# Optimization experiments

Hardware: AMD Instinct MI355X
Metric: run time of the kernel (lower is better)

Reference implementation:

```python
import jax, jax.numpy as jnp
import numpy as np

N = 262144
D = 3            # n_dims
G = 128          # n_gaussians
F = 128          # n_features
L = 8            # num_positional_encoding_terms
H = 512          # nodes_per_layer
OUT = 1          # n_outputs
PE_DIM = L * 2 * D  # 48
IN0 = PE_DIM + F    # 176


def setup_inputs() -> dict:
    key = jax.random.key(0)
    ks = jax.random.split(key, 16)
    x = jax.random.uniform(ks[0], (N, D), dtype=jnp.float32) * 2.0 - 1.0
    centers = jax.random.uniform(ks[1], (G, D), dtype=jnp.float32) * 2.0 - 1.0
    # diagonal covariances (as in the torch init: eye * rand), kept well-conditioned
    diag = 0.05 + 0.1 * jax.random.uniform(ks[2], (G, D), dtype=jnp.float32)
    cov = jax.vmap(jnp.diag)(diag)  # [G, D, D]
    bnd = np.sqrt(6.0 / F) / 30.0
    gfeat = jax.random.uniform(ks[3], (G, F), dtype=jnp.float32, minval=-bnd, maxval=bnd)

    def lin(kw, kb, fan_out, fan_in, scale):
        W = jax.random.uniform(kw, (fan_out, fan_in), dtype=jnp.float32, minval=-scale, maxval=scale)
        b = jax.random.uniform(kb, (fan_out,), dtype=jnp.float32, minval=-scale, maxval=scale)
        return W, b

    W1, b1 = lin(ks[4], ks[5], H, IN0, float(np.sqrt(6.0 / IN0)))          # LReLU layer
    sine_s = float(np.sqrt(6.0 / H) / 30.0)
    W2, b2 = lin(ks[6], ks[7], H, H, sine_s)
    W3, b3 = lin(ks[8], ks[9], H, H, sine_s)
    W4, b4 = lin(ks[10], ks[11], H, H, sine_s)
    W5, b5 = lin(ks[12], ks[13], OUT, H, float(np.sqrt(2.0 / (H + OUT))))  # final linear
    return {"x": x, "centers": centers, "cov": cov, "gfeat": gfeat,
            "W1": W1, "b1": b1, "W2": W2, "b2": b2, "W3": W3, "b3": b3,
            "W4": W4, "b4": b4, "W5": W5, "b5": b5}


def _positional_encoding(x):
    # torch layout: for each freq l, [sin(2^l*pi*x), sin(..y), sin(..z), cos(..x), cos(..y), cos(..z)]
    freqs = (2.0 ** jnp.arange(L, dtype=jnp.float32)) * jnp.pi  # [L]
    s = x[:, None, :] * freqs[None, :, None]                    # [N, L, D]
    pe = jnp.concatenate([jnp.sin(s), jnp.cos(s)], axis=-1)     # [N, L, 2D]
    return pe.reshape(x.shape[0], L * 2 * D)


def reference(x, centers, cov, gfeat, W1, b1, W2, b2, W3, b3, W4, b4, W5, b5):
    pe = _positional_encoding(x)                                # [N, 48]
    # Gaussian mixture density per point per gaussian
    inv = jnp.linalg.inv(cov)                                   # [G, D, D]
    det = jnp.linalg.det(cov)                                   # [G]
    coeff = 1.0 / (((2.0 * jnp.pi) ** (D / 2.0)) * jnp.sqrt(det))  # [G]
    diff = x[:, None, :] - centers[None, :, :]                  # [N, G, D]
    maha = jnp.einsum('ngd,gde,nge->ng', diff, inv, diff)       # [N, G]
    dens = coeff[None, :] * jnp.exp(-0.5 * maha)                # [N, G]
    feat = dens @ gfeat                                         # [N, F]
    h = jnp.concatenate([feat, pe], axis=1)                     # [N, 176]
    h = jax.nn.leaky_relu(h @ W1.T + b1, 0.2)
    h = jnp.sin(30.0 * (h @ W2.T + b2))
    h = jnp.sin(30.0 * (h @ W3.T + b3))
    h = jnp.sin(30.0 * (h @ W4.T + b4))
    return h @ W5.T + b5                                        # [N, 1]
```

## Files before the change

kernel.cpp:

```cpp
#include <hip/hip_runtime.h>

typedef __attribute__((ext_vector_type(8))) short bf16x8;
typedef __attribute__((ext_vector_type(4))) float f32x4;

#define NPTS 262144
#define PTS_PER_BLK 128
#define TPB 512

__device__ __forceinline__ unsigned short f2bf(float f) {
  unsigned int u = __float_as_uint(f);
  u += 0x7fffu + ((u >> 16) & 1u);
  return (unsigned short)(u >> 16);
}
__device__ __forceinline__ float bf2f(unsigned short s) {
  return __uint_as_float(((unsigned int)s) << 16);
}

__global__ void prep_w(const float* __restrict__ src, unsigned short* __restrict__ dst,
                       int KIN, int KB, int trans, int OUTD, int total) {
  int idx = blockIdx.x * blockDim.x + threadIdx.x;
  if (idx >= total) return;
  int i = idx & 7;
  int l = (idx >> 3) & 63;
  int t = idx >> 9;
  int kb = t % KB, nb = t / KB;
  int row = nb * 16 + (l & 15);
  int k = kb * 32 + (l >> 4) * 8 + i;
  float v = 0.0f;
  if (k < KIN) v = trans ? src[k * OUTD + row] : src[row * KIN + k];
  dst[idx] = f2bf(v);
}

__global__ void prep_gauss(const float* __restrict__ centers, const float* __restrict__ cov,
                           float* __restrict__ gp) {
  int g = threadIdx.x;
  if (g >= 128) return;
  float c0 = cov[g * 9 + 0], c1 = cov[g * 9 + 4], c2 = cov[g * 9 + 8];
  float det = c0 * c1 * c2;
  float coeff = 1.0f / (15.749609945722419f * sqrtf(det));
  gp[g * 8 + 0] = centers[g * 3 + 0];
  gp[g * 8 + 1] = centers[g * 3 + 1];
  gp[g * 8 + 2] = centers[g * 3 + 2];
  gp[g * 8 + 3] = 1.0f / c0;
  gp[g * 8 + 4] = 1.0f / c1;
  gp[g * 8 + 5] = 1.0f / c2;
  gp[g * 8 + 6] = coeff;
  gp[g * 8 + 7] = 0.0f;
}


template <int KB, int ACT>
__device__ __forceinline__ void mlp_layer(const unsigned short* __restrict__ wf,
                                          const float* __restrict__ bias,
                                          char* hb, int lane, int wid) {
  const int r8 = lane >> 4, l15 = lane & 15;
  f32x4 acc[4][8];
#pragma unroll
  for (int a0 = 0; a0 < 4; ++a0)
#pragma unroll
    for (int b0 = 0; b0 < 8; ++b0)
      acc[a0][b0] = (f32x4){0.f, 0.f, 0.f, 0.f};

  const unsigned short* wbase = wf + wid * 4 * KB * 512 + lane * 8;
#pragma unroll 4
  for (int kb = 0; kb < KB; ++kb) {
    bf16x8 a[4];
#pragma unroll
    for (int nf = 0; nf < 4; ++nf)
      a[nf] = *(const bf16x8*)(wbase + (nf * KB + kb) * 512);
    bf16x8 b[8];
#pragma unroll
    for (int pf = 0; pf < 8; ++pf) {
      int pt = pf * 16 + l15;
      int off = (pt * 1024 + kb * 64 + r8 * 16) ^ ((pt & 7) << 4);
      b[pf] = *(const bf16x8*)(hb + off);
    }
#pragma unroll
    for (int nf = 0; nf < 4; ++nf)
#pragma unroll
      for (int pf = 0; pf < 8; ++pf)
        acc[nf][pf] = __builtin_amdgcn_mfma_f32_16x16x32_bf16(a[nf], b[pf], acc[nf][pf], 0, 0, 0);
  }
  __syncthreads();
#pragma unroll
  for (int nf = 0; nf < 4; ++nf) {
    int n0 = wid * 64 + nf * 16 + r8 * 4;
    f32x4 bv = *(const f32x4*)(bias + n0);
#pragma unroll
    for (int pf = 0; pf < 8; ++pf) {
      int pt = pf * 16 + l15;
      float v[4];
#pragma unroll
      for (int r = 0; r < 4; ++r) {
        float z = acc[nf][pf][r] + bv[r];
        if (ACT == 1) z = (z > 0.f) ? z : 0.2f * z;
        else if (ACT == 2) z = __sinf(30.f * z);
        v[r] = z;
      }
      unsigned long long pk =
          (unsigned long long)((unsigned int)f2bf(v[0]) | ((unsigned int)f2bf(v[1]) << 16)) |
          ((unsigned long long)((unsigned int)f2bf(v[2]) | ((unsigned int)f2bf(v[3]) << 16)) << 32);
      int off = (pt * 1024 + n0 * 2) ^ ((pt & 7) << 4);
      *(unsigned long long*)(hb + off) = pk;
    }
  }
  __syncthreads();
}

__global__ __launch_bounds__(TPB, 2) void gmminr_main(
    const float* __restrict__ x,
    const float* __restrict__ b1, const float* __restrict__ b2,
    const float* __restrict__ b3, const float* __restrict__ b4,
    const float* __restrict__ w5, const float* __restrict__ b5,
    const unsigned short* __restrict__ wf1, const unsigned short* __restrict__ wf2,
    const unsigned short* __restrict__ wf3, const unsigned short* __restrict__ wf4,
    const unsigned short* __restrict__ gff, const float* __restrict__ gp,
    float* __restrict__ out) {
  __shared__ char hb[PTS_PER_BLK * 1024];
  const int tid = threadIdx.x;
  const int lane = tid & 63;
  const int wid = tid >> 6;
  const int pt0 = blockIdx.x * PTS_PER_BLK;

  {
    const int pt = tid >> 2;
    const int q = tid & 3;
    const float X = x[(pt0 + pt) * 3 + 0];
    const float Y = x[(pt0 + pt) * 3 + 1];
    const float Z = x[(pt0 + pt) * 3 + 2];
#pragma unroll 2
    for (int j = 0; j < 32; j += 4) {
      float d4[4];
#pragma unroll
      for (int e = 0; e < 4; ++e) {
        const float* P = gp + (q * 32 + j + e) * 8;
        float dx = X - P[0], dy = Y - P[1], dz = Z - P[2];
        float m = dx * dx * P[3] + dy * dy * P[4] + dz * dz * P[5];
        d4[e] = P[6] * __expf(-0.5f * m);
      }
      unsigned long long pk =
          (unsigned long long)((unsigned int)f2bf(d4[0]) | ((unsigned int)f2bf(d4[1]) << 16)) |
          ((unsigned long long)((unsigned int)f2bf(d4[2]) | ((unsigned int)f2bf(d4[3]) << 16)) << 32);
      int col = 256 + q * 32 + j;
      int off = (pt * 1024 + col * 2) ^ ((pt & 7) << 4);
      *(unsigned long long*)(hb + off) = pk;
    }
    float co[3] = {X, Y, Z};
#pragma unroll
    for (int lg = 0; lg < 2; ++lg) {
      int le = q * 2 + lg;
      float fr = 3.14159265358979323846f * (float)(1 << le);
#pragma unroll
      for (int d = 0; d < 3; ++d) {
        float arg = fr * co[d];
        float s = __sinf(arg), c = __cosf(arg);
        int cs = 128 + le * 6 + d;
        *(unsigned short*)(hb + ((pt * 1024 + cs * 2) ^ ((pt & 7) << 4))) = f2bf(s);
        *(unsigned short*)(hb + ((pt * 1024 + (cs + 3) * 2) ^ ((pt & 7) << 4))) = f2bf(c);
      }
    }
    {
      int col = 176 + q * 4;
      int off = (pt * 1024 + col * 2) ^ ((pt & 7) << 4);
      *(unsigned long long*)(hb + off) = 0ull;
    }
  }
  __syncthreads();

  {
    const int r8 = lane >> 4, l15 = lane & 15;
    f32x4 facc[8];
#pragma unroll
    for (int pf = 0; pf < 8; ++pf) facc[pf] = (f32x4){0.f, 0.f, 0.f, 0.f};
    const unsigned short* gbase = gff + wid * 4 * 512 + lane * 8;
#pragma unroll
    for (int kb = 0; kb < 4; ++kb) {
      bf16x8 a = *(const bf16x8*)(gbase + kb * 512);
#pragma unroll
      for (int pf = 0; pf < 8; ++pf) {
        int pt = pf * 16 + l15;
        int off = (pt * 1024 + 512 + kb * 64 + r8 * 16) ^ ((pt & 7) << 4);
        bf16x8 b = *(const bf16x8*)(hb + off);
        facc[pf] = __builtin_amdgcn_mfma_f32_16x16x32_bf16(a, b, facc[pf], 0, 0, 0);
      }
    }
    int f0 = wid * 16 + r8 * 4;
#pragma unroll
    for (int pf = 0; pf < 8; ++pf) {
      int pt = pf * 16 + l15;
      unsigned long long pk =
          (unsigned long long)((unsigned int)f2bf(facc[pf][0]) | ((unsigned int)f2bf(facc[pf][1]) << 16)) |
          ((unsigned long long)((unsigned int)f2bf(facc[pf][2]) | ((unsigned int)f2bf(facc[pf][3]) << 16)) << 32);
      int off = (pt * 1024 + f0 * 2) ^ ((pt & 7) << 4);
      *(unsigned long long*)(hb + off) = pk;
    }
  }
  __syncthreads();

  mlp_layer<6, 1>(wf1, b1, hb, lane, wid);
  mlp_layer<16, 2>(wf2, b2, hb, lane, wid);
  mlp_layer<16, 2>(wf3, b3, hb, lane, wid);
  mlp_layer<16, 2>(wf4, b4, hb, lane, wid);

  {
    const int pt = tid >> 2, q = tid & 3;
    float s = 0.f;
#pragma unroll 4
    for (int kk = 0; kk < 128; kk += 8) {
      int k = q * 128 + kk;
      int off = (pt * 1024 + k * 2) ^ ((pt & 7) << 4);
      bf16x8 hv = *(const bf16x8*)(hb + off);
      f32x4 w0 = *(const f32x4*)(w5 + k);
      f32x4 w1 = *(const f32x4*)(w5 + k + 4);
#pragma unroll
      for (int e = 0; e < 4; ++e) s += bf2f((unsigned short)hv[e]) * w0[e];
#pragma unroll
      for (int e = 0; e < 4; ++e) s += bf2f((unsigned short)hv[4 + e]) * w1[e];
    }
    s += __shfl_down(s, 2, 4);
    s += __shfl_down(s, 1, 4);
    if (q == 0) out[pt0 + pt] = s + b5[0];
  }
}

extern "C" void kernel_launch(void* const* d_in, const int* in_sizes, int n_in,
                              void* d_out, int out_size, void* d_ws, size_t ws_size,
                              hipStream_t stream) {
  const float* x   = (const float*)d_in[0];
  const float* cen = (const float*)d_in[1];
  const float* cov = (const float*)d_in[2];
  const float* gfe = (const float*)d_in[3];
  const float* W1  = (const float*)d_in[4];
  const float* b1  = (const float*)d_in[5];
  const float* W2  = (const float*)d_in[6];
  const float* b2  = (const float*)d_in[7];
  const float* W3  = (const float*)d_in[8];
  const float* b3  = (const float*)d_in[9];
  const float* W4  = (const float*)d_in[10];
  const float* b4  = (const float*)d_in[11];
  const float* W5  = (const float*)d_in[12];
  const float* b5  = (const float*)d_in[13];
  float* out = (float*)d_out;

  char* ws = (char*)d_ws;
  unsigned short* wf1 = (unsigned short*)(ws);
  unsigned short* wf2 = (unsigned short*)(ws + 196608);
  unsigned short* wf3 = (unsigned short*)(ws + 720896);
  unsigned short* wf4 = (unsigned short*)(ws + 1245184);
  unsigned short* gff = (unsigned short*)(ws + 1769472);
  float* gp = (float*)(ws + 1802240);

  prep_w<<<98304 / 256, 256, 0, stream>>>(W1, wf1, 176, 6, 0, 512, 98304);
  prep_w<<<262144 / 256, 256, 0, stream>>>(W2, wf2, 512, 16, 0, 512, 262144);
  prep_w<<<262144 / 256, 256, 0, stream>>>(W3, wf3, 512, 16, 0, 512, 262144);
  prep_w<<<262144 / 256, 256, 0, stream>>>(W4, wf4, 512, 16, 0, 512, 262144);
  prep_w<<<16384 / 256, 256, 0, stream>>>(gfe, gff, 128, 4, 1, 128, 16384);
  prep_gauss<<<1, 128, 0, stream>>>(cen, cov, gp);

  gmminr_main<<<NPTS / PTS_PER_BLK, TPB, 0, stream>>>(
      x, b1, b2, b3, b4, W5, b5, wf1, wf2, wf3, wf4, gff, gp, out);
}
```

Before: 678.0 us.

## Halve points per block, raise occupancy, fuse last sine layer with output

```diff
diff --git a/kernel.cpp b/kernel.cpp
--- a/kernel.cpp
+++ b/kernel.cpp
@@ -4,16 +4,20 @@
 typedef __attribute__((ext_vector_type(4))) float f32x4;
 
 #define NPTS 262144
-#define PTS_PER_BLK 128
+#define PTS_PER_BLK 64
 #define TPB 512
+#define NBLK (NPTS / PTS_PER_BLK)
 
 __device__ __forceinline__ unsigned short f2bf(float f) {
   unsigned int u = __float_as_uint(f);
   u += 0x7fffu + ((u >> 16) & 1u);
   return (unsigned short)(u >> 16);
 }
-__device__ __forceinline__ float bf2f(unsigned short s) {
-  return __uint_as_float(((unsigned int)s) << 16);
+__device__ __forceinline__ unsigned int pklo(float a, float b) {
+  return (unsigned int)f2bf(a) | ((unsigned int)f2bf(b) << 16);
+}
+__device__ __forceinline__ unsigned long long pk4(float a, float b, float c, float d) {
+  return (unsigned long long)pklo(a, b) | ((unsigned long long)pklo(c, d) << 32);
 }
 
 __global__ void prep_w(const float* __restrict__ src, unsigned short* __restrict__ dst,
@@ -48,29 +52,34 @@
   gp[g * 8 + 7] = 0.0f;
 }
 
+__global__ void prep_scale(const float* __restrict__ src, float* __restrict__ dst, int n) {
+  int i = blockIdx.x * blockDim.x + threadIdx.x;
+  if (i < n) dst[i] = src[i] * 30.0f;
+}
+
 
 template <int KB, int ACT>
 __device__ __forceinline__ void mlp_layer(const unsigned short* __restrict__ wf,
                                           const float* __restrict__ bias,
                                           char* hb, int lane, int wid) {
   const int r8 = lane >> 4, l15 = lane & 15;
-  f32x4 acc[4][8];
+  f32x4 acc[4][4];
 #pragma unroll
   for (int a0 = 0; a0 < 4; ++a0)
 #pragma unroll
-    for (int b0 = 0; b0 < 8; ++b0)
+    for (int b0 = 0; b0 < 4; ++b0)
       acc[a0][b0] = (f32x4){0.f, 0.f, 0.f, 0.f};
 
   const unsigned short* wbase = wf + wid * 4 * KB * 512 + lane * 8;
-#pragma unroll 4
+#pragma unroll 2
   for (int kb = 0; kb < KB; ++kb) {
     bf16x8 a[4];
 #pragma unroll
     for (int nf = 0; nf < 4; ++nf)
       a[nf] = *(const bf16x8*)(wbase + (nf * KB + kb) * 512);
-    bf16x8 b[8];
-#pragma unroll
-    for (int pf = 0; pf < 8; ++pf) {
+    bf16x8 b[4];
+#pragma unroll
+    for (int pf = 0; pf < 4; ++pf) {
       int pt = pf * 16 + l15;
       int off = (pt * 1024 + kb * 64 + r8 * 16) ^ ((pt & 7) << 4);
       b[pf] = *(const bf16x8*)(hb + off);
@@ -78,7 +87,7 @@
 #pragma unroll
     for (int nf = 0; nf < 4; ++nf)
 #pragma unroll
-      for (int pf = 0; pf < 8; ++pf)
+      for (int pf = 0; pf < 4; ++pf)
         acc[nf][pf] = __builtin_amdgcn_mfma_f32_16x16x32_bf16(a[nf], b[pf], acc[nf][pf], 0, 0, 0);
   }
   __syncthreads();
@@ -87,97 +96,81 @@
     int n0 = wid * 64 + nf * 16 + r8 * 4;
     f32x4 bv = *(const f32x4*)(bias + n0);
 #pragma unroll
-    for (int pf = 0; pf < 8; ++pf) {
+    for (int pf = 0; pf < 4; ++pf) {
       int pt = pf * 16 + l15;
-      float v[4];
+      float z[4];
 #pragma unroll
       for (int r = 0; r < 4; ++r) {
-        float z = acc[nf][pf][r] + bv[r];
-        if (ACT == 1) z = (z > 0.f) ? z : 0.2f * z;
-        else if (ACT == 2) z = __sinf(30.f * z);
-        v[r] = z;
-      }
-      unsigned long long pk =
-          (unsigned long long)((unsigned int)f2bf(v[0]) | ((unsigned int)f2bf(v[1]) << 16)) |
-          ((unsigned long long)((unsigned int)f2bf(v[2]) | ((unsigned int)f2bf(v[3]) << 16)) << 32);
+        float t = acc[nf][pf][r];
+        if (ACT == 1) { t += bv[r]; t = t > 0.f ? t : 0.2f * t; }
+        else { t = __sinf(fmaf(t, 30.0f, bv[r])); }
+        z[r] = t;
+      }
       int off = (pt * 1024 + n0 * 2) ^ ((pt & 7) << 4);
-      *(unsigned long long*)(hb + off) = pk;
-    }
-  }
-  __syncthreads();
-}
-
-__global__ __launch_bounds__(TPB, 2) void gmminr_main(
+      *(unsigned long long*)(hb + off) = pk4(z[0], z[1], z[2], z[3]);
+    }
+  }
+  __syncthreads();
+}
+
+__global__ __launch_bounds__(TPB, 4) void gmminr_main(
     const float* __restrict__ x,
-    const float* __restrict__ b1, const float* __restrict__ b2,
-    const float* __restrict__ b3, const float* __restrict__ b4,
+    const float* __restrict__ b1, const float* __restrict__ bs2,
+    const float* __restrict__ bs3, const float* __restrict__ bs4,
     const float* __restrict__ w5, const float* __restrict__ b5,
     const unsigned short* __restrict__ wf1, const unsigned short* __restrict__ wf2,
     const unsigned short* __restrict__ wf3, const unsigned short* __restrict__ wf4,
     const unsigned short* __restrict__ gff, const float* __restrict__ gp,
     float* __restrict__ out) {
-  __shared__ char hb[PTS_PER_BLK * 1024];
+  __shared__ char hb[PTS_PER_BLK * 1024 + 2048];
+  float* part = (float*)(hb + PTS_PER_BLK * 1024);
   const int tid = threadIdx.x;
   const int lane = tid & 63;
   const int wid = tid >> 6;
+  const int r8 = lane >> 4, l15 = lane & 15;
   const int pt0 = blockIdx.x * PTS_PER_BLK;
 
   {
-    const int pt = tid >> 2;
-    const int q = tid & 3;
-    const float X = x[(pt0 + pt) * 3 + 0];
-    const float Y = x[(pt0 + pt) * 3 + 1];
-    const float Z = x[(pt0 + pt) * 3 + 2];
-#pragma unroll 2
-    for (int j = 0; j < 32; j += 4) {
+    const int pt = tid >> 3;
+    const int q = tid & 7;
+    const int gpt = pt0 + pt;
+    const float X = x[gpt * 3 + 0], Y = x[gpt * 3 + 1], Z = x[gpt * 3 + 2];
+    const int ps = (pt & 7) << 4;
+    const int pb = pt * 1024;
+#pragma unroll
+    for (int j = 0; j < 16; j += 4) {
       float d4[4];
 #pragma unroll
       for (int e = 0; e < 4; ++e) {
-        const float* P = gp + (q * 32 + j + e) * 8;
+        const float* P = gp + (q * 16 + j + e) * 8;
         float dx = X - P[0], dy = Y - P[1], dz = Z - P[2];
-        float m = dx * dx * P[3] + dy * dy * P[4] + dz * dz * P[5];
+        float m = fmaf(dx * dx, P[3], fmaf(dy * dy, P[4], dz * dz * P[5]));
         d4[e] = P[6] * __expf(-0.5f * m);
       }
-      unsigned long long pk =
-          (unsigned long long)((unsigned int)f2bf(d4[0]) | ((unsigned int)f2bf(d4[1]) << 16)) |
-          ((unsigned long long)((unsigned int)f2bf(d4[2]) | ((unsigned int)f2bf(d4[3]) << 16)) << 32);
-      int col = 256 + q * 32 + j;
-      int off = (pt * 1024 + col * 2) ^ ((pt & 7) << 4);
-      *(unsigned long long*)(hb + off) = pk;
-    }
-    float co[3] = {X, Y, Z};
-#pragma unroll
-    for (int lg = 0; lg < 2; ++lg) {
-      int le = q * 2 + lg;
-      float fr = 3.14159265358979323846f * (float)(1 << le);
-#pragma unroll
-      for (int d = 0; d < 3; ++d) {
-        float arg = fr * co[d];
-        float s = __sinf(arg), c = __cosf(arg);
-        int cs = 128 + le * 6 + d;
-        *(unsigned short*)(hb + ((pt * 1024 + cs * 2) ^ ((pt & 7) << 4))) = f2bf(s);
-        *(unsigned short*)(hb + ((pt * 1024 + (cs + 3) * 2) ^ ((pt & 7) << 4))) = f2bf(c);
-      }
-    }
-    {
-      int col = 176 + q * 4;
-      int off = (pt * 1024 + col * 2) ^ ((pt & 7) << 4);
-      *(unsigned long long*)(hb + off) = 0ull;
-    }
+      int off = (pb + 512 + q * 32 + j * 2) ^ ps;
+      *(unsigned long long*)(hb + off) = pk4(d4[0], d4[1], d4[2], d4[3]);
+    }
+    float fr = 3.14159265358979323846f * (float)(1 << q);
+    float sx = __sinf(fr * X), sy = __sinf(fr * Y), sz2 = __sinf(fr * Z);
+    float cx = __cosf(fr * X), cy = __cosf(fr * Y), cz = __cosf(fr * Z);
+    int base = pb + 256 + 12 * q;
+    *(unsigned int*)(hb + ((base + 0) ^ ps)) = pklo(sx, sy);
+    *(unsigned int*)(hb + ((base + 4) ^ ps)) = pklo(sz2, cx);
+    *(unsigned int*)(hb + ((base + 8) ^ ps)) = pklo(cy, cz);
+    *(unsigned int*)(hb + ((pb + 352 + 4 * q) ^ ps)) = 0u;
   }
   __syncthreads();
 
   {
-    const int r8 = lane >> 4, l15 = lane & 15;
-    f32x4 facc[8];
-#pragma unroll
-    for (int pf = 0; pf < 8; ++pf) facc[pf] = (f32x4){0.f, 0.f, 0.f, 0.f};
+    f32x4 facc[4];
+#pragma unroll
+    for (int pf = 0; pf < 4; ++pf) facc[pf] = (f32x4){0.f, 0.f, 0.f, 0.f};
     const unsigned short* gbase = gff + wid * 4 * 512 + lane * 8;
 #pragma unroll
     for (int kb = 0; kb < 4; ++kb) {
       bf16x8 a = *(const bf16x8*)(gbase + kb * 512);
 #pragma unroll
-      for (int pf = 0; pf < 8; ++pf) {
+      for (int pf = 0; pf < 4; ++pf) {
         int pt = pf * 16 + l15;
         int off = (pt * 1024 + 512 + kb * 64 + r8 * 16) ^ ((pt & 7) << 4);
         bf16x8 b = *(const bf16x8*)(hb + off);
@@ -186,40 +179,64 @@
     }
     int f0 = wid * 16 + r8 * 4;
 #pragma unroll
-    for (int pf = 0; pf < 8; ++pf) {
+    for (int pf = 0; pf < 4; ++pf) {
       int pt = pf * 16 + l15;
-      unsigned long long pk =
-          (unsigned long long)((unsigned int)f2bf(facc[pf][0]) | ((unsigned int)f2bf(facc[pf][1]) << 16)) |
-          ((unsigned long long)((unsigned int)f2bf(facc[pf][2]) | ((unsigned int)f2bf(facc[pf][3]) << 16)) << 32);
       int off = (pt * 1024 + f0 * 2) ^ ((pt & 7) << 4);
-      *(unsigned long long*)(hb + off) = pk;
+      *(unsigned long long*)(hb + off) = pk4(facc[pf][0], facc[pf][1], facc[pf][2], facc[pf][3]);
     }
   }
   __syncthreads();
 
   mlp_layer<6, 1>(wf1, b1, hb, lane, wid);
-  mlp_layer<16, 2>(wf2, b2, hb, lane, wid);
-  mlp_layer<16, 2>(wf3, b3, hb, lane, wid);
-  mlp_layer<16, 2>(wf4, b4, hb, lane, wid);
+  mlp_layer<16, 2>(wf2, bs2, hb, lane, wid);
+  mlp_layer<16, 2>(wf3, bs3, hb, lane, wid);
 
   {
-    const int pt = tid >> 2, q = tid & 3;
-    float s = 0.f;
-#pragma unroll 4
-    for (int kk = 0; kk < 128; kk += 8) {
-      int k = q * 128 + kk;
-      int off = (pt * 1024 + k * 2) ^ ((pt & 7) << 4);
-      bf16x8 hv = *(const bf16x8*)(hb + off);
-      f32x4 w0 = *(const f32x4*)(w5 + k);
-      f32x4 w1 = *(const f32x4*)(w5 + k + 4);
-#pragma unroll
-      for (int e = 0; e < 4; ++e) s += bf2f((unsigned short)hv[e]) * w0[e];
-#pragma unroll
-      for (int e = 0; e < 4; ++e) s += bf2f((unsigned short)hv[4 + e]) * w1[e];
-    }
-    s += __shfl_down(s, 2, 4);
-    s += __shfl_down(s, 1, 4);
-    if (q == 0) out[pt0 + pt] = s + b5[0];
+    f32x4 acc[4][4];
+#pragma unroll
+    for (int a0 = 0; a0 < 4; ++a0)
+#pragma unroll
+      for (int b0 = 0; b0 < 4; ++b0)
+        acc[a0][b0] = (f32x4){0.f, 0.f, 0.f, 0.f};
+    const unsigned short* wbase = wf4 + wid * 4 * 16 * 512 + lane * 8;
+#pragma unroll 2
+    for (int kb = 0; kb < 16; ++kb) {
+      bf16x8 a[4];
+#pragma unroll
+      for (int nf = 0; nf < 4; ++nf)
+        a[nf] = *(const bf16x8*)(wbase + (nf * 16 + kb) * 512);
+#pragma unroll
+      for (int pf = 0; pf < 4; ++pf) {
+        int pt = pf * 16 + l15;
+        int off = (pt * 1024 + kb * 64 + r8 * 16) ^ ((pt & 7) << 4);
+        bf16x8 b = *(const bf16x8*)(hb + off);
+#pragma unroll
+        for (int nf = 0; nf < 4; ++nf)
+          acc[nf][pf] = __builtin_amdgcn_mfma_f32_16x16x32_bf16(a[nf], b, acc[nf][pf], 0, 0, 0);
+      }
+    }
+#pragma unroll
+    for (int pf = 0; pf < 4; ++pf) {
+      float s = 0.f;
+#pragma unroll
+      for (int nf = 0; nf < 4; ++nf) {
+        int n0 = wid * 64 + nf * 16 + r8 * 4;
+        f32x4 bv = *(const f32x4*)(bs4 + n0);
+        f32x4 wv = *(const f32x4*)(w5 + n0);
+#pragma unroll
+        for (int r = 0; r < 4; ++r)
+          s += __sinf(fmaf(acc[nf][pf][r], 30.0f, bv[r])) * wv[r];
+      }
+      s += __shfl_xor(s, 16);
+      s += __shfl_xor(s, 32);
+      if (lane < 16) part[(pf * 16 + l15) * 8 + wid] = s;
+    }
+  }
+  __syncthreads();
+  if (tid < PTS_PER_BLK) {
+    const f32x4* pp = (const f32x4*)part;
+    f32x4 a = pp[tid * 2], b = pp[tid * 2 + 1];
+    out[pt0 + tid] = a[0] + a[1] + a[2] + a[3] + b[0] + b[1] + b[2] + b[3] + b5[0];
   }
 }
 
@@ -248,15 +265,21 @@
   unsigned short* wf3 = (unsigned short*)(ws + 720896);
   unsigned short* wf4 = (unsigned short*)(ws + 1245184);
   unsigned short* gff = (unsigned short*)(ws + 1769472);
-  float* gp = (float*)(ws + 1802240);
-
-  prep_w<<<98304 / 256, 256, 0, stream>>>(W1, wf1, 176, 6, 0, 512, 98304);
-  prep_w<<<262144 / 256, 256, 0, stream>>>(W2, wf2, 512, 16, 0, 512, 262144);
-  prep_w<<<262144 / 256, 256, 0, stream>>>(W3, wf3, 512, 16, 0, 512, 262144);
-  prep_w<<<262144 / 256, 256, 0, stream>>>(W4, wf4, 512, 16, 0, 512, 262144);
-  prep_w<<<16384 / 256, 256, 0, stream>>>(gfe, gff, 128, 4, 1, 128, 16384);
+  float* gp  = (float*)(ws + 1802240);
+  float* bs2 = (float*)(ws + 1806336);
+  float* bs3 = (float*)(ws + 1808384);
+  float* bs4 = (float*)(ws + 1810432);
+
+  prep_w<<<384, 256, 0, stream>>>(W1, wf1, 176, 6, 0, 512, 98304);
+  prep_w<<<1024, 256, 0, stream>>>(W2, wf2, 512, 16, 0, 512, 262144);
+  prep_w<<<1024, 256, 0, stream>>>(W3, wf3, 512, 16, 0, 512, 262144);
+  prep_w<<<1024, 256, 0, stream>>>(W4, wf4, 512, 16, 0, 512, 262144);
+  prep_w<<<64, 256, 0, stream>>>(gfe, gff, 128, 4, 1, 128, 16384);
   prep_gauss<<<1, 128, 0, stream>>>(cen, cov, gp);
-
-  gmminr_main<<<NPTS / PTS_PER_BLK, TPB, 0, stream>>>(
-      x, b1, b2, b3, b4, W5, b5, wf1, wf2, wf3, wf4, gff, gp, out);
-}
+  prep_scale<<<2, 256, 0, stream>>>(b2, bs2, 512);
+  prep_scale<<<2, 256, 0, stream>>>(b3, bs3, 512);
+  prep_scale<<<2, 256, 0, stream>>>(b4, bs4, 512);
+
+  gmminr_main<<<NBLK, TPB, 0, stream>>>(x, b1, bs2, bs3, bs4, W5, b5,
+                                        wf1, wf2, wf3, wf4, gff, gp, out);
+}
```

Result: faster. 582.8 us (-14.0%).
